# Performance work log

Hardware: AMD Instinct MI355X
Metric: run time of the kernel (lower is better)

The kernel has to match this reference:

```python
import jax, jax.numpy as jnp
import numpy as np

T, B, D, H = 8192, 4, 1024, 16  # seq_len, batch, d_model, n_heads


def setup_inputs() -> dict:
    key = jax.random.key(0)
    k1, k2, k3 = jax.random.split(key, 3)
    s = 1.0 / np.sqrt(D).astype(np.float32)
    return {
        "query": jax.random.normal(k1, (T, B, D), jnp.float32),
        "Wqkv": jax.random.normal(k2, (3 * D, D), jnp.float32) * s,
        "bqkv": jnp.zeros((3 * D,), jnp.float32),
        "Wout": jax.random.normal(k3, (D, D), jnp.float32) * s,
        "bout": jnp.zeros((D,), jnp.float32),
    }


def reference(query, Wqkv, bqkv, Wout, bout):
    Tl, Bs, Dm = query.shape
    hd = Dm // H
    # fused qkv projection: [T,B,3D]
    qkv = query @ Wqkv.T + bqkv
    q, k, v = jnp.split(qkv, 3, axis=-1)

    def heads(x):
        # torch: view(T, B*H, hd).transpose(0,1).view(B,H,T,hd)
        return x.reshape(Tl, Bs, H, hd).transpose(1, 2, 0, 3)  # [B,H,T,hd]

    qh, kh, vh = heads(q), heads(k), heads(v)

    # corrcoef over head_dim axis, T is the sample axis: X,Y are [B,H,hd,T]
    X = jnp.swapaxes(qh, -1, -2)
    Y = jnp.swapaxes(kh, -1, -2)
    Xc = X - X.mean(-1, keepdims=True)
    Yc = Y - Y.mean(-1, keepdims=True)
    c = jnp.einsum('bhiT,bhjT->bhij', Xc, Yc)          # [B,H,hd,hd] covariance
    sx = (Xc * Xc).sum(-1, keepdims=True)              # [B,H,hd,1]
    sy = (Yc * Yc).sum(-1)[..., None, :]               # [B,H,1,hd]
    corr = jnp.clip(c / jnp.sqrt(sx * sy), 0.0, 1.0)
    corr = jax.nn.softmax(corr, axis=-2)               # softmax over rows (dim=-2)

    # weighted sum: v @ corr  -> [B,H,T,hd]
    attn = jnp.einsum('bhtd,bhde->bhte', vh, corr)
    # permute(2,0,1,3).view(T*B, D) then out_proj then view(T,B,D)
    out = attn.transpose(2, 0, 1, 3).reshape(Tl * Bs, Dm) @ Wout.T + bout
    return out.reshape(Tl, Bs, Dm)
```

## Files before the change

### kernel.cpp

```cpp
#include <hip/hip_runtime.h>
#include <stdint.h>


typedef unsigned short u16;
typedef __attribute__((ext_vector_type(8))) short bf16x8;
typedef __attribute__((ext_vector_type(8))) u16  u16x8;
typedef __attribute__((ext_vector_type(4))) float f32x4;

#define AS1 __attribute__((address_space(1)))
#define AS3 __attribute__((address_space(3)))

__device__ __forceinline__ u16 f2b(float f) {
  union { float f; uint32_t u; } x; x.f = f;
  const uint32_t u = x.u;
  return (u16)((u + 0x7FFFu + ((u >> 16) & 1u)) >> 16);
}
__device__ __forceinline__ void g2l16(const void* g, void* l) {
  __builtin_amdgcn_global_load_lds((const AS1 uint32_t*)g, (AS3 uint32_t*)l, 16, 0, 0);
}

__global__ __launch_bounds__(256) void cvt_all(
    const float* __restrict__ q, const float* __restrict__ w1, const float* __restrict__ w2,
    u16* __restrict__ qb, u16* __restrict__ w1b, u16* __restrict__ w2b)
{
  int i = blockIdx.x * 256 + threadIdx.x;
  if (i >= 4718592) return;
  const float* s; u16* d; int ofs;
  if (i < 4194304)      { s = q;  d = qb;  ofs = i; }
  else if (i < 4587520) { s = w1; d = w1b; ofs = i - 4194304; }
  else                  { s = w2; d = w2b; ofs = i - 4587520; }
  const float4 a = *(const float4*)(s + (size_t)ofs * 8);
  const float4 b = *(const float4*)(s + (size_t)ofs * 8 + 4);
  u16x8 o;
  o[0] = f2b(a.x); o[1] = f2b(a.y); o[2] = f2b(a.z); o[3] = f2b(a.w);
  o[4] = f2b(b.x); o[5] = f2b(b.y); o[6] = f2b(b.z); o[7] = f2b(b.w);
  *(u16x8*)(d + (size_t)ofs * 8) = o;
}

__global__ __launch_bounds__(256) void gemm_qk(
    const u16* __restrict__ W, const u16* __restrict__ Q,
    const float* __restrict__ bias, u16* __restrict__ qkT)
{
  __shared__ __align__(16) u16 As[128 * 64];
  __shared__ __align__(16) u16 Bs[128 * 64];
  const int tid = threadIdx.x;
  const int bn = blockIdx.x & 63;
  const int bm = (blockIdx.x >> 6) & 15;
  const int b  = blockIdx.x >> 10;
  const int m0 = bm * 128, n0 = bn * 128;
  const int lane = tid & 63, wave = tid >> 6;
  const int wm = (wave >> 1) * 64, wn = (wave & 1) * 64;
  const int laneN = lane & 15, laneQ = lane >> 4;

  const int srow = tid >> 3;
  const int skb  = (tid & 7) ^ (srow & 7);
  const u16* gA = W + (size_t)(m0 + srow) * 1024 + skb * 8;
  const u16* gB = Q + ((size_t)(n0 + srow) * 4 + b) * 1024 + skb * 8;
  u16* lA = &As[tid * 8];
  u16* lB = &Bs[tid * 8];

  f32x4 acc[4][4] = {};

  for (int kt = 0; kt < 1024; kt += 64) {
    __syncthreads();
#pragma unroll
    for (int i = 0; i < 4; ++i) {
      g2l16(gA + kt + (size_t)(i * 32) * 1024, lA + i * 2048);
      g2l16(gB + kt + (size_t)(i * 32) * 4096, lB + i * 2048);
    }
    __syncthreads();
#pragma unroll
    for (int ks2 = 0; ks2 < 2; ++ks2) {
      bf16x8 af[4], bf[4];
#pragma unroll
      for (int i = 0; i < 4; ++i) {
        const int row = wm + i * 16 + laneN;
        const int kq  = (ks2 * 4 + laneQ) ^ (row & 7);
        af[i] = *(const bf16x8*)&As[row * 64 + kq * 8];
      }
#pragma unroll
      for (int j = 0; j < 4; ++j) {
        const int row = wn + j * 16 + laneN;
        const int kq  = (ks2 * 4 + laneQ) ^ (row & 7);
        bf[j] = *(const bf16x8*)&Bs[row * 64 + kq * 8];
      }
#pragma unroll
      for (int i = 0; i < 4; ++i)
#pragma unroll
        for (int j = 0; j < 4; ++j)
          acc[i][j] = __builtin_amdgcn_mfma_f32_16x16x32_bf16(af[i], bf[j], acc[i][j], 0, 0, 0);
    }
  }

#pragma unroll
  for (int i = 0; i < 4; ++i) {
#pragma unroll
    for (int r = 0; r < 4; ++r) {
      const int f = m0 + wm + i * 16 + laneQ * 4 + r;
      const float bv = bias[f];
      const int seg = f >> 10, h = (f & 1023) >> 6, d = f & 63;
      u16* base = qkT + (size_t)seg * 33554432 +
                  ((size_t)((b * 16 + h) * 64 + d)) * 8192;
#pragma unroll
      for (int j = 0; j < 4; ++j) {
        const int t = n0 + wn + j * 16 + laneN;
        base[t] = f2b(acc[i][j][r] + bv);
      }
    }
  }
}

template <int MODE>
__global__ __launch_bounds__(256) void gemm_bt(
    const u16* __restrict__ A, const u16* __restrict__ Bw,
    const float* __restrict__ bias, void* __restrict__ OutP,
    int M, int N, int K, int nTilesN)
{
  __shared__ __align__(16) u16 As[128 * 64];
  __shared__ __align__(16) u16 Bs[128 * 64];
  const int tid = threadIdx.x;
  const int bn = blockIdx.x % nTilesN;
  const int bm = blockIdx.x / nTilesN;
  const int m0 = bm * 128, n0 = bn * 128;
  const int lane = tid & 63, wave = tid >> 6;
  const int wm = (wave >> 1) * 64, wn = (wave & 1) * 64;
  const int laneN = lane & 15, laneQ = lane >> 4;

  const int srow = tid >> 3;
  const int skb  = (tid & 7) ^ (srow & 7);
  const u16* gA = A  + (size_t)(m0 + srow) * K + skb * 8;
  const u16* gB = Bw + (size_t)(n0 + srow) * K + skb * 8;
  u16* lA = &As[tid * 8];
  u16* lB = &Bs[tid * 8];

  f32x4 acc[4][4] = {};

  for (int kt = 0; kt < K; kt += 64) {
    __syncthreads();
#pragma unroll
    for (int i = 0; i < 4; ++i) {
      g2l16(gA + kt + (size_t)(i * 32) * K, lA + i * 2048);
      g2l16(gB + kt + (size_t)(i * 32) * K, lB + i * 2048);
    }
    __syncthreads();
#pragma unroll
    for (int ks2 = 0; ks2 < 2; ++ks2) {
      bf16x8 af[4], bf[4];
#pragma unroll
      for (int i = 0; i < 4; ++i) {
        const int row = wm + i * 16 + laneN;
        const int kq  = (ks2 * 4 + laneQ) ^ (row & 7);
        af[i] = *(const bf16x8*)&As[row * 64 + kq * 8];
      }
#pragma unroll
      for (int j = 0; j < 4; ++j) {
        const int row = wn + j * 16 + laneN;
        const int kq  = (ks2 * 4 + laneQ) ^ (row & 7);
        bf[j] = *(const bf16x8*)&Bs[row * 64 + kq * 8];
      }
#pragma unroll
      for (int i = 0; i < 4; ++i)
#pragma unroll
        for (int j = 0; j < 4; ++j)
          acc[i][j] = __builtin_amdgcn_mfma_f32_16x16x32_bf16(af[i], bf[j], acc[i][j], 0, 0, 0);
    }
  }

#pragma unroll
  for (int i = 0; i < 4; ++i) {
#pragma unroll
    for (int j = 0; j < 4; ++j) {
      const int col = n0 + wn + j * 16 + laneN;
      const float bv = bias[col];
#pragma unroll
      for (int r = 0; r < 4; ++r) {
        const int row = m0 + wm + i * 16 + laneQ * 4 + r;
        const float v = acc[i][j][r] + bv;
        if (MODE == 0) ((u16*)OutP)[(size_t)row * N + col] = f2b(v);
        else           ((float*)OutP)[(size_t)row * N + col] = v;
      }
    }
  }
}

__global__ __launch_bounds__(256) void stats_k(
    const u16* __restrict__ qT, const u16* __restrict__ kT,
    float* __restrict__ Spart, float* __restrict__ Mpart)
{
  __shared__ __align__(16) u16 smem[2 * 4 * 64 * 64];
  __shared__ float margLDS[4 * 256];
  u16* Qs = smem;
  u16* Ks = smem + 16384;
  const int tid = threadIdx.x;
  const int bh = blockIdx.x & 63;
  const int chunk = blockIdx.x >> 6;
  const int t0 = chunk * 1024;
  const int lane = tid & 63, wave = tid >> 6;
  const int laneN = lane & 15, laneQ = lane >> 4;

  const u16* qp = qT + (size_t)bh * 524288;
  const u16* kp = kT + (size_t)bh * 524288;

  f32x4 accS[4][4] = {};
  f32x4 accQQ[4] = {}, accKK[4] = {}, accQ1[4] = {}, accK1[4] = {};
  bf16x8 ones;
#pragma unroll
  for (int j = 0; j < 8; ++j) ones[j] = (short)0x3F80;

  for (int rd = 0; rd < 4; ++rd) {
    __syncthreads();
#pragma unroll
    for (int i = 0; i < 8; ++i) {
      const int c = tid + i * 256;
      const int tile = c >> 9, cw = c & 511;
      const int d = cw >> 3, slot = cw & 7;
      const int kb = slot ^ (d & 7);
      const size_t gofs = (size_t)d * 8192 + (t0 + rd * 256 + tile * 64 + kb * 8);
      g2l16(qp + gofs, &Qs[c * 8]);
      g2l16(kp + gofs, &Ks[c * 8]);
    }
    __syncthreads();
    const u16* qt = &Qs[wave * 4096];
    const u16* kt2 = &Ks[wave * 4096];
#pragma unroll
    for (int ks2 = 0; ks2 < 2; ++ks2) {
      bf16x8 qf[4], kf[4];
#pragma unroll
      for (int i = 0; i < 4; ++i) {
        const int d = i * 16 + laneN;
        const int kq = (ks2 * 4 + laneQ) ^ (d & 7);
        qf[i] = *(const bf16x8*)&qt[d * 64 + kq * 8];
        kf[i] = *(const bf16x8*)&kt2[d * 64 + kq * 8];
      }
#pragma unroll
      for (int i = 0; i < 4; ++i) {
#pragma unroll
        for (int j = 0; j < 4; ++j)
          accS[i][j] = __builtin_amdgcn_mfma_f32_16x16x32_bf16(qf[i], kf[j], accS[i][j], 0, 0, 0);
        accQQ[i] = __builtin_amdgcn_mfma_f32_16x16x32_bf16(qf[i], qf[i], accQQ[i], 0, 0, 0);
        accKK[i] = __builtin_amdgcn_mfma_f32_16x16x32_bf16(kf[i], kf[i], accKK[i], 0, 0, 0);
        accQ1[i] = __builtin_amdgcn_mfma_f32_16x16x32_bf16(qf[i], ones, accQ1[i], 0, 0, 0);
        accK1[i] = __builtin_amdgcn_mfma_f32_16x16x32_bf16(kf[i], ones, accK1[i], 0, 0, 0);
      }
    }
  }

  __syncthreads();
  float* red = (float*)smem;
#pragma unroll
  for (int i = 0; i < 4; ++i)
#pragma unroll
    for (int j = 0; j < 4; ++j)
#pragma unroll
      for (int r = 0; r < 4; ++r) {
        const int d = i * 16 + laneQ * 4 + r, e = j * 16 + laneN;
        red[wave * 4096 + d * 64 + e] = accS[i][j][r];
      }
#pragma unroll
  for (int i = 0; i < 4; ++i) {
    if (laneN == 0) {
#pragma unroll
      for (int r = 0; r < 4; ++r) {
        const int d = i * 16 + laneQ * 4 + r;
        margLDS[wave * 256 + 0 * 64 + d] = accQ1[i][r];
        margLDS[wave * 256 + 2 * 64 + d] = accK1[i][r];
      }
    }
    if ((laneN >> 2) == laneQ) {
      const int r = laneN & 3;
      const int d = i * 16 + laneN;
      margLDS[wave * 256 + 1 * 64 + d] = accQQ[i][r];
      margLDS[wave * 256 + 3 * 64 + d] = accKK[i][r];
    }
  }
  __syncthreads();
  float* Sp = Spart + ((size_t)chunk * 64 + bh) * 4096;
  for (int c = tid; c < 4096; c += 256)
    Sp[c] = red[c] + red[4096 + c] + red[8192 + c] + red[12288 + c];
  float* Mp = Mpart + ((size_t)chunk * 64 + bh) * 256;
  Mp[tid] = margLDS[tid] + margLDS[256 + tid] + margLDS[512 + tid] + margLDS[768 + tid];
}

__global__ __launch_bounds__(64) void finalize_k(
    const float* __restrict__ Spart, const float* __restrict__ Mpart,
    u16* __restrict__ corrT)
{
  __shared__ float Ss[4096];
  __shared__ float sqs[64], sxs[64];
  const int bh = blockIdx.x;
  const int e = threadIdx.x;
  for (int idx = e; idx < 4096; idx += 64) {
    float s = 0.f;
#pragma unroll
    for (int c = 0; c < 8; ++c) s += Spart[((size_t)c * 64 + bh) * 4096 + idx];
    Ss[idx] = s;
  }
  float m[4];
#pragma unroll
  for (int p = 0; p < 4; ++p) {
    float s = 0.f;
#pragma unroll
    for (int c = 0; c < 8; ++c) s += Mpart[((size_t)c * 64 + bh) * 256 + p * 64 + e];
    m[p] = s;
  }
  const float invT = 1.0f / 8192.0f;
  const float sy = m[3] - m[2] * m[2] * invT;
  const float ske = m[2];
  sqs[e] = m[0];
  sxs[e] = m[1] - m[0] * m[0] * invT;
  __syncthreads();
  float mx = 0.0f;
  for (int d = 0; d < 64; ++d) {
    const float c = Ss[d * 64 + e] - sqs[d] * ske * invT;
    float r = c / sqrtf(sxs[d] * sy);
    r = fminf(fmaxf(r, 0.0f), 1.0f);
    Ss[d * 64 + e] = r;
    mx = fmaxf(mx, r);
  }
  float sum = 0.f;
  for (int d = 0; d < 64; ++d) {
    const float ev = expf(Ss[d * 64 + e] - mx);
    Ss[d * 64 + e] = ev;
    sum += ev;
  }
  const float inv = 1.0f / sum;
  for (int d = 0; d < 64; ++d)
    corrT[(size_t)bh * 4096 + e * 64 + d] = f2b(Ss[d * 64 + e] * inv);
}

__global__ __launch_bounds__(256) void attn_k(
    const u16* __restrict__ vb, const u16* __restrict__ corrT,
    u16* __restrict__ attnb)
{
  __shared__ __align__(16) u16 Vs[256 * 64];
  __shared__ __align__(16) u16 Cs[64 * 64];
  const int tid = threadIdx.x;
  const int bh = blockIdx.x & 63;
  const int tt0 = (blockIdx.x >> 6) * 256;
  const int b = bh >> 4, h = bh & 15;
  const int lane = tid & 63, wave = tid >> 6;
  const int laneN = lane & 15, laneQ = lane >> 4;

  {
#pragma unroll
    for (int i = 0; i < 8; ++i) {
      const int c = tid + i * 256;
      const int row = c >> 3, slot = c & 7;
      const int kb = slot ^ (row & 7);
      const u16* g = vb + (size_t)((tt0 + row) * 4 + b) * 1024 + h * 64 + kb * 8;
      g2l16(g, &Vs[c * 8]);
    }
#pragma unroll
    for (int i = 0; i < 2; ++i) {
      const int c = tid + i * 256;
      const int row = c >> 3, slot = c & 7;
      const int kb = slot ^ (row & 7);
      g2l16(corrT + (size_t)bh * 4096 + row * 64 + kb * 8, &Cs[c * 8]);
    }
  }
  __syncthreads();

  const int wt = wave * 64;
  f32x4 acc[4][4] = {};
#pragma unroll
  for (int ks2 = 0; ks2 < 2; ++ks2) {
    bf16x8 af[4], bf[4];
#pragma unroll
    for (int i = 0; i < 4; ++i) {
      const int row = wt + i * 16 + laneN;
      const int kq = (ks2 * 4 + laneQ) ^ (row & 7);
      af[i] = *(const bf16x8*)&Vs[row * 64 + kq * 8];
    }
#pragma unroll
    for (int j = 0; j < 4; ++j) {
      const int row = j * 16 + laneN;
      const int kq = (ks2 * 4 + laneQ) ^ (row & 7);
      bf[j] = *(const bf16x8*)&Cs[row * 64 + kq * 8];
    }
#pragma unroll
    for (int i = 0; i < 4; ++i)
#pragma unroll
      for (int j = 0; j < 4; ++j)
        acc[i][j] = __builtin_amdgcn_mfma_f32_16x16x32_bf16(af[i], bf[j], acc[i][j], 0, 0, 0);
  }
#pragma unroll
  for (int i = 0; i < 4; ++i)
#pragma unroll
    for (int j = 0; j < 4; ++j)
#pragma unroll
      for (int r = 0; r < 4; ++r) {
        const int t = tt0 + wt + i * 16 + laneQ * 4 + r;
        const int e = j * 16 + laneN;
        attnb[(size_t)(t * 4 + b) * 1024 + h * 64 + e] = f2b(acc[i][j][r]);
      }
}

extern "C" void kernel_launch(void* const* d_in, const int* in_sizes, int n_in,
                              void* d_out, int out_size, void* d_ws, size_t ws_size,
                              hipStream_t stream)
{
  const float* query = (const float*)d_in[0];
  const float* Wqkv  = (const float*)d_in[1];
  const float* bqkv  = (const float*)d_in[2];
  const float* Wout  = (const float*)d_in[3];
  const float* bout  = (const float*)d_in[4];
  char* ws = (char*)d_ws;

  u16*   qkT    = (u16*)(ws);
  u16*   kT     = (u16*)(ws + 67108864);
  u16*   vb     = (u16*)(ws + 134217728);
  u16*   queryb = (u16*)(ws + 201326592);
  float* Spart  = (float*)(ws + 201326592);
  float* Mpart  = (float*)(ws + 209715200);
  u16*   corrT  = (u16*)(ws + 210239488);
  u16*   Wqkvb  = (u16*)(ws + 268435456);
  u16*   Woutb  = (u16*)(ws + 274726912);

  cvt_all<<<dim3(18432), dim3(256), 0, stream>>>(query, Wqkv, Wout, queryb, Wqkvb, Woutb);

  gemm_qk<<<dim3(4096), dim3(256), 0, stream>>>(Wqkvb, queryb, bqkv, qkT);
  gemm_bt<0><<<dim3(2048), dim3(256), 0, stream>>>(queryb, Wqkvb + (size_t)2048 * 1024,
                                                   bqkv + 2048, vb, 32768, 1024, 1024, 8);
  stats_k<<<dim3(512), dim3(256), 0, stream>>>(qkT, kT, Spart, Mpart);
  finalize_k<<<dim3(64), dim3(64), 0, stream>>>(Spart, Mpart, corrT);
  attn_k<<<dim3(2048), dim3(256), 0, stream>>>(vb, corrT, qkT);
  gemm_bt<2><<<dim3(2048), dim3(256), 0, stream>>>(qkT, Woutb, bout, d_out,
                                                   32768, 1024, 1024, 8);
}
```

Baseline: 671.0 us.

## Replace GEMMs with 256x256 tile, 8-wave, double-buffered pipelined MFMA kernel

Replaces the three 128x128 single-buffered GEMM kernels with one templated kernel that uses 256x256 tiles, 512 threads (8 waves) and double-buffered LDS. Global-to-LDS loads for later k-halves are issued in between MFMA phases, with vmcnt waits and raw barriers replacing the full __syncthreads pairs. It also raises MFMA priority with setprio during compute. The goal is to hide load latency and improve data reuse per tile, at the cost of more registers and LDS per block and fewer blocks in the grid.

```diff
diff --git a/kernel.cpp b/kernel.cpp
--- a/kernel.cpp
+++ b/kernel.cpp
@@ -37,151 +37,150 @@
   *(u16x8*)(d + (size_t)ofs * 8) = o;
 }
 
-__global__ __launch_bounds__(256) void gemm_qk(
-    const u16* __restrict__ W, const u16* __restrict__ Q,
-    const float* __restrict__ bias, u16* __restrict__ qkT)
-{
-  __shared__ __align__(16) u16 As[128 * 64];
-  __shared__ __align__(16) u16 Bs[128 * 64];
+#define BARX() do { asm volatile("" ::: "memory");                    \
+                    __builtin_amdgcn_s_barrier();                     \
+                    asm volatile("" ::: "memory"); } while (0)
+
+#define LOADA(KH, MH)                                                 \
+  _Pragma("unroll") for (int m_ = 0; m_ < 4; ++m_) {                  \
+    const int row_ = wr * 128 + (MH) * 64 + m_ * 16 + laneN;          \
+    const int sl_ = laneQ ^ ((row_ >> 1) & 3);                        \
+    af[m_] = *(const bf16x8*)&As[buf_][KH][row_ * 32 + sl_ * 8];      \
+  }
+
+#define LOADB(KH)                                                     \
+  _Pragma("unroll") for (int n_ = 0; n_ < 4; ++n_) {                  \
+    const int row_ = wc * 64 + n_ * 16 + laneN;                       \
+    const int sl_ = laneQ ^ ((row_ >> 1) & 3);                        \
+    bf[n_] = *(const bf16x8*)&Bs[buf_][KH][row_ * 32 + sl_ * 8];      \
+  }
+
+#define MFMA16(MH)                                                    \
+  __builtin_amdgcn_s_setprio(1);                                      \
+  _Pragma("unroll") for (int m_ = 0; m_ < 4; ++m_)                    \
+    _Pragma("unroll") for (int n_ = 0; n_ < 4; ++n_)                  \
+      acc[(MH) * 4 + m_][n_] = __builtin_amdgcn_mfma_f32_16x16x32_bf16( \
+          af[m_], bf[n_], acc[(MH) * 4 + m_][n_], 0, 0, 0);           \
+  __builtin_amdgcn_s_setprio(0);
+
+#define GTILE(T, TAILWAIT) do {                                       \
+    const int buf_ = (T) & 1;                                         \
+    bf16x8 af[4], bf[4];                                              \
+    LOADA(0, 0) LOADB(0)                                              \
+    issue_half(4 * (T) + 6);                                          \
+    BARX(); MFMA16(0); BARX();                                        \
+    LOADA(0, 1)                                                       \
+    issue_half(4 * (T) + 7);                                          \
+    BARX(); MFMA16(1); BARX();                                        \
+    LOADA(1, 0) LOADB(1)                                              \
+    issue_half(4 * (T) + 8);                                          \
+    BARX(); MFMA16(0); BARX();                                        \
+    LOADA(1, 1)                                                       \
+    issue_half(4 * (T) + 9);                                          \
+    BARX(); MFMA16(1);                                                \
+    TAILWAIT;                                                         \
+    BARX();                                                           \
+  } while (0)
+
+template <int MODE>
+__global__ __launch_bounds__(512, 2) void gemm8p(
+    const u16* __restrict__ A, const u16* __restrict__ B,
+    const float* __restrict__ bias, void* __restrict__ OutP)
+{
+  __shared__ __align__(16) u16 As[2][2][8192];
+  __shared__ __align__(16) u16 Bs[2][2][8192];
   const int tid = threadIdx.x;
-  const int bn = blockIdx.x & 63;
-  const int bm = (blockIdx.x >> 6) & 15;
-  const int b  = blockIdx.x >> 10;
-  const int m0 = bm * 128, n0 = bn * 128;
+  int bn, bm, batch;
+  if (MODE == 0) { bn = blockIdx.x & 31; bm = (blockIdx.x >> 5) & 7; batch = blockIdx.x >> 8; }
+  else           { bn = blockIdx.x & 3;  bm = blockIdx.x >> 2;       batch = 0; }
+  const int m0 = bm * 256, n0 = bn * 256;
   const int lane = tid & 63, wave = tid >> 6;
-  const int wm = (wave >> 1) * 64, wn = (wave & 1) * 64;
+  const int wr = wave >> 2, wc = wave & 3;
   const int laneN = lane & 15, laneQ = lane >> 4;
 
-  const int srow = tid >> 3;
-  const int skb  = (tid & 7) ^ (srow & 7);
-  const u16* gA = W + (size_t)(m0 + srow) * 1024 + skb * 8;
-  const u16* gB = Q + ((size_t)(n0 + srow) * 4 + b) * 1024 + skb * 8;
-  u16* lA = &As[tid * 8];
-  u16* lB = &Bs[tid * 8];
-
-  f32x4 acc[4][4] = {};
-
-  for (int kt = 0; kt < 1024; kt += 64) {
-    __syncthreads();
-#pragma unroll
-    for (int i = 0; i < 4; ++i) {
-      g2l16(gA + kt + (size_t)(i * 32) * 1024, lA + i * 2048);
-      g2l16(gB + kt + (size_t)(i * 32) * 4096, lB + i * 2048);
-    }
-    __syncthreads();
-#pragma unroll
-    for (int ks2 = 0; ks2 < 2; ++ks2) {
-      bf16x8 af[4], bf[4];
-#pragma unroll
-      for (int i = 0; i < 4; ++i) {
-        const int row = wm + i * 16 + laneN;
-        const int kq  = (ks2 * 4 + laneQ) ^ (row & 7);
-        af[i] = *(const bf16x8*)&As[row * 64 + kq * 8];
-      }
-#pragma unroll
-      for (int j = 0; j < 4; ++j) {
-        const int row = wn + j * 16 + laneN;
-        const int kq  = (ks2 * 4 + laneQ) ^ (row & 7);
-        bf[j] = *(const bf16x8*)&Bs[row * 64 + kq * 8];
-      }
-#pragma unroll
-      for (int i = 0; i < 4; ++i)
-#pragma unroll
-        for (int j = 0; j < 4; ++j)
-          acc[i][j] = __builtin_amdgcn_mfma_f32_16x16x32_bf16(af[i], bf[j], acc[i][j], 0, 0, 0);
-    }
-  }
-
-#pragma unroll
-  for (int i = 0; i < 4; ++i) {
-#pragma unroll
-    for (int r = 0; r < 4; ++r) {
-      const int f = m0 + wm + i * 16 + laneQ * 4 + r;
-      const float bv = bias[f];
-      const int seg = f >> 10, h = (f & 1023) >> 6, d = f & 63;
-      u16* base = qkT + (size_t)seg * 33554432 +
-                  ((size_t)((b * 16 + h) * 64 + d)) * 8192;
-#pragma unroll
-      for (int j = 0; j < 4; ++j) {
-        const int t = n0 + wn + j * 16 + laneN;
-        base[t] = f2b(acc[i][j][r] + bv);
-      }
-    }
-  }
-}
-
-template <int MODE>
-__global__ __launch_bounds__(256) void gemm_bt(
-    const u16* __restrict__ A, const u16* __restrict__ Bw,
-    const float* __restrict__ bias, void* __restrict__ OutP,
-    int M, int N, int K, int nTilesN)
-{
-  __shared__ __align__(16) u16 As[128 * 64];
-  __shared__ __align__(16) u16 Bs[128 * 64];
-  const int tid = threadIdx.x;
-  const int bn = blockIdx.x % nTilesN;
-  const int bm = blockIdx.x / nTilesN;
-  const int m0 = bm * 128, n0 = bn * 128;
-  const int lane = tid & 63, wave = tid >> 6;
-  const int wm = (wave >> 1) * 64, wn = (wave & 1) * 64;
-  const int laneN = lane & 15, laneQ = lane >> 4;
-
-  const int srow = tid >> 3;
-  const int skb  = (tid & 7) ^ (srow & 7);
-  const u16* gA = A  + (size_t)(m0 + srow) * K + skb * 8;
-  const u16* gB = Bw + (size_t)(n0 + srow) * K + skb * 8;
-  u16* lA = &As[tid * 8];
-  u16* lB = &Bs[tid * 8];
-
-  f32x4 acc[4][4] = {};
-
-  for (int kt = 0; kt < K; kt += 64) {
-    __syncthreads();
-#pragma unroll
-    for (int i = 0; i < 4; ++i) {
-      g2l16(gA + kt + (size_t)(i * 32) * K, lA + i * 2048);
-      g2l16(gB + kt + (size_t)(i * 32) * K, lB + i * 2048);
-    }
-    __syncthreads();
-#pragma unroll
-    for (int ks2 = 0; ks2 < 2; ++ks2) {
-      bf16x8 af[4], bf[4];
-#pragma unroll
-      for (int i = 0; i < 4; ++i) {
-        const int row = wm + i * 16 + laneN;
-        const int kq  = (ks2 * 4 + laneQ) ^ (row & 7);
-        af[i] = *(const bf16x8*)&As[row * 64 + kq * 8];
-      }
-#pragma unroll
-      for (int j = 0; j < 4; ++j) {
-        const int row = wn + j * 16 + laneN;
-        const int kq  = (ks2 * 4 + laneQ) ^ (row & 7);
-        bf[j] = *(const bf16x8*)&Bs[row * 64 + kq * 8];
-      }
-#pragma unroll
-      for (int i = 0; i < 4; ++i)
-#pragma unroll
-        for (int j = 0; j < 4; ++j)
-          acc[i][j] = __builtin_amdgcn_mfma_f32_16x16x32_bf16(af[i], bf[j], acc[i][j], 0, 0, 0);
-    }
-  }
-
-#pragma unroll
-  for (int i = 0; i < 4; ++i) {
-#pragma unroll
-    for (int j = 0; j < 4; ++j) {
-      const int col = n0 + wn + j * 16 + laneN;
-      const float bv = bias[col];
+  const u16* Abase = A + (size_t)m0 * 1024;
+  const size_t bPitch = (MODE == 0) ? 4096 : 1024;
+  const u16* Bbase = (MODE == 0) ? (B + (size_t)batch * 1024 + (size_t)n0 * 4096)
+                                 : (B + (size_t)n0 * 1024);
+
+  const int sr = tid >> 2, sl = tid & 3;
+  const int qg = sl ^ ((sr >> 1) & 3);
+  const size_t aofs0 = (size_t)sr * 1024 + qg * 8;
+  const size_t aofs1 = aofs0 + (size_t)128 * 1024;
+  const size_t bofs0 = (size_t)sr * bPitch + qg * 8;
+  const size_t bofs1 = bofs0 + (size_t)128 * bPitch;
+
+  auto issue_half = [&](int q) {
+    if (q >= 64) return;
+    const int tq = q >> 2, ty = q & 3;
+    const int bufq = tq & 1, kh = ty >> 1;
+    const int kofs = tq * 64 + kh * 32;
+    if ((ty & 1) == 0) {
+      u16* l = &As[bufq][kh][tid * 8];
+      g2l16(Abase + aofs0 + kofs, l);
+      g2l16(Abase + aofs1 + kofs, l + 4096);
+    } else {
+      u16* l = &Bs[bufq][kh][tid * 8];
+      g2l16(Bbase + bofs0 + kofs, l);
+      g2l16(Bbase + bofs1 + kofs, l + 4096);
+    }
+  };
+
+  f32x4 acc[8][4] = {};
+
+#pragma unroll
+  for (int q = 0; q < 6; ++q) issue_half(q);
+  asm volatile("s_waitcnt vmcnt(4)" ::: "memory");
+  __builtin_amdgcn_s_barrier();
+  asm volatile("" ::: "memory");
+
+#pragma unroll 2
+  for (int t = 0; t < 14; ++t)
+    GTILE(t, asm volatile("s_waitcnt vmcnt(4)" ::: "memory"));
+  GTILE(14, asm volatile("s_waitcnt vmcnt(0)" ::: "memory"));
+  GTILE(15, (void)0);
+
+  if (MODE == 0) {
+#pragma unroll
+    for (int m = 0; m < 8; ++m) {
 #pragma unroll
       for (int r = 0; r < 4; ++r) {
-        const int row = m0 + wm + i * 16 + laneQ * 4 + r;
-        const float v = acc[i][j][r] + bv;
-        if (MODE == 0) ((u16*)OutP)[(size_t)row * N + col] = f2b(v);
-        else           ((float*)OutP)[(size_t)row * N + col] = v;
-      }
-    }
-  }
-}
+        const int f = m0 + wr * 128 + m * 16 + laneQ * 4 + r;
+        const float bv = bias[f];
+        const int seg = f >> 10, h = (f & 1023) >> 6, d = f & 63;
+        u16* base = (u16*)OutP + (size_t)seg * 33554432 +
+                    ((size_t)((batch * 16 + h) * 64 + d)) * 8192;
+#pragma unroll
+        for (int n = 0; n < 4; ++n) {
+          const int t = n0 + wc * 64 + n * 16 + laneN;
+          base[t] = f2b(acc[m][n][r] + bv);
+        }
+      }
+    }
+  } else {
+#pragma unroll
+    for (int m = 0; m < 8; ++m) {
+#pragma unroll
+      for (int n = 0; n < 4; ++n) {
+        const int col = n0 + wc * 64 + n * 16 + laneN;
+        const float bv = bias[col];
+#pragma unroll
+        for (int r = 0; r < 4; ++r) {
+          const int row = m0 + wr * 128 + m * 16 + laneQ * 4 + r;
+          const float v = acc[m][n][r] + bv;
+          if (MODE == 1) ((u16*)OutP)[(size_t)row * 1024 + col] = f2b(v);
+          else           ((float*)OutP)[(size_t)row * 1024 + col] = v;
+        }
+      }
+    }
+  }
+}
+
+#undef GTILE
+#undef MFMA16
+#undef LOADB
+#undef LOADA
+#undef BARX
 
 __global__ __launch_bounds__(256) void stats_k(
     const u16* __restrict__ qT, const u16* __restrict__ kT,
@@ -418,12 +417,11 @@
 
   cvt_all<<<dim3(18432), dim3(256), 0, stream>>>(query, Wqkv, Wout, queryb, Wqkvb, Woutb);
 
-  gemm_qk<<<dim3(4096), dim3(256), 0, stream>>>(Wqkvb, queryb, bqkv, qkT);
-  gemm_bt<0><<<dim3(2048), dim3(256), 0, stream>>>(queryb, Wqkvb + (size_t)2048 * 1024,
-                                                   bqkv + 2048, vb, 32768, 1024, 1024, 8);
+  gemm8p<0><<<dim3(1024), dim3(512), 0, stream>>>(Wqkvb, queryb, bqkv, qkT);
+  gemm8p<1><<<dim3(512), dim3(512), 0, stream>>>(queryb, Wqkvb + (size_t)2048 * 1024,
+                                                 bqkv + 2048, vb);
   stats_k<<<dim3(512), dim3(256), 0, stream>>>(qkT, kT, Spart, Mpart);
   finalize_k<<<dim3(64), dim3(64), 0, stream>>>(Spart, Mpart, corrT);
   attn_k<<<dim3(2048), dim3(256), 0, stream>>>(vb, corrT, qkT);
-  gemm_bt<2><<<dim3(2048), dim3(256), 0, stream>>>(qkT, Woutb, bout, d_out,
-                                                   32768, 1024, 1024, 8);
-}
+  gemm8p<2><<<dim3(512), dim3(512), 0, stream>>>(qkT, Woutb, bout, d_out);
+}
```

Result: faster. 639.4 us (-4.7%).
